# Performance work log

Hardware: AMD Instinct MI355X
Metric: run time of the kernel (lower is better)

Reference implementation:

```python
import jax, jax.numpy as jnp
import numpy as np

# Uniform ragged-segment sizes (ptr[i] = i * size)
B = 1024    # num graphs in batch
NT = 128    # tasks per graph
NV = 128    # vehicles per graph
NR = 16     # RSUs per graph
D = 64      # embed_dim
H = 32      # power-head hidden
NTGT = NR + NV
NEG = -1e9  # masked_fill value from the torch code


def setup_inputs() -> dict:
    key = jax.random.key(0)
    ks = jax.random.split(key, 10)
    return {
        "task_node_emb": jax.random.normal(ks[0], (B * NT, D), jnp.float32),
        "task_global_emb": jax.random.normal(ks[1], (B, D), jnp.float32),
        "veh_emb": jax.random.normal(ks[2], (B * NV, D), jnp.float32),
        "rsu_emb": jax.random.normal(ks[3], (B * NR, D), jnp.float32),
        "task_mask": jax.random.randint(ks[4], (B * NT,), 0, 2).astype(bool),
        "target_mask": jax.random.randint(ks[5], (B * NT, NTGT), 0, 2).astype(bool),
        "W1": jax.random.normal(ks[6], (2 * D, H), jnp.float32) * 0.1,
        "b1": jnp.zeros((H,), jnp.float32),
        "W2": jax.random.normal(ks[7], (H, 1), jnp.float32) * 0.1,
        "b2": jnp.zeros((1,), jnp.float32),
    }


def reference(task_node_emb, task_global_emb, veh_emb, rsu_emb,
              task_mask, target_mask, W1, b1, W2, b2):
    # Reshape flat ragged storage into uniform per-graph segments
    t = task_node_emb.reshape(B, NT, D)
    v = veh_emb.reshape(B, NV, D)
    r = rsu_emb.reshape(B, NR, D)

    # targets = cat([rsu, veh]) per graph; scores = task @ targets^T / sqrt(D)
    targets = jnp.concatenate([r, v], axis=1)              # [B, NTGT, D]
    scores = jnp.einsum('btd,bkd->btk', t, targets) / jnp.sqrt(jnp.float32(D))

    # masked_fill(~task_mask.unsqueeze(1), -1e9)
    tm = task_mask.reshape(B, NT, 1)
    scores = jnp.where(tm, scores, NEG)
    # masked_fill(~target_mask, -1e9) (same fill value, order irrelevant)
    tg = target_mask.reshape(B, NT, NTGT)
    scores = jnp.where(tg, scores, NEG)

    # flatten per graph; uniform lengths => pad_sequence is a no-op reshape
    padded_logits = scores.reshape(B, NT * NTGT)

    # power head on [task_global ; first vehicle emb of each graph]
    p_feat = jnp.concatenate([task_global_emb, v[:, 0, :]], axis=1)  # [B, 2D]
    h = jax.nn.relu(p_feat @ W1 + b1)
    power = jax.nn.sigmoid(h @ W2 + b2)                    # [B, 1]

    return padded_logits, power
```

## Files before the change

kernel.cpp:

```cpp
#include <hip/hip_runtime.h>

#define NB      1024
#define NT_     128
#define NV_     128
#define NR_     16
#define D_      64
#define H_      32
#define NTGT_   144
#define SCG     18432
#define PWR_OFF 18874368
#define NEGV    (-1e9f)
#define EPAD    148
#define EWAVE   (8 * EPAD)
#define NSB     2048

typedef __attribute__((ext_vector_type(8))) short  short8;
typedef __attribute__((ext_vector_type(4))) float  floatx4;

__device__ __forceinline__ unsigned int f2bf_pack(float lo, float hi) {
    unsigned int ul = __float_as_uint(lo);
    ul += 0x7FFFu + ((ul >> 16) & 1u);
    unsigned int uh = __float_as_uint(hi);
    uh += 0x7FFFu + ((uh >> 16) & 1u);
    return (ul >> 16) | (uh & 0xFFFF0000u);
}

extern "C" __global__ void __launch_bounds__(256, 8)
thy_fused(const float* __restrict__ tEmb,
          const float* __restrict__ gEmb,
          const float* __restrict__ vEmb,
          const float* __restrict__ rEmb,
          const int* __restrict__ tMask,
          const int* __restrict__ gMask,
          const float* __restrict__ W1,
          const float* __restrict__ b1,
          const float* __restrict__ W2,
          const float* __restrict__ b2,
          float* __restrict__ out)
{
    __shared__ __align__(16) unsigned char smem[18944];
    const int tid = threadIdx.x;
    const int blk = blockIdx.x;

    if (blk < NSB) {
        const int b    = blk >> 1;
        const int half = blk & 1;
        const int lane = tid & 63;
        const int w    = tid >> 6;
        const int ln   = lane & 15;
        const int kg   = lane >> 4;

        const float* arow_p = tEmb + ((size_t)b * NT_ + half * 64 + w * 16 + ln) * D_;
        float4 fa0 = *(const float4*)(arow_p + kg * 8);
        float4 fa1 = *(const float4*)(arow_p + kg * 8 + 4);
        float4 fb0 = *(const float4*)(arow_p + 32 + kg * 8);
        float4 fb1 = *(const float4*)(arow_p + 32 + kg * 8 + 4);

        {
            const float4* rs = (const float4*)(rEmb + (size_t)b * (NR_ * D_));
            const float4* vs = (const float4*)(vEmb + (size_t)b * (NV_ * D_));
            #pragma unroll
            for (int it = 0; it < 9; ++it) {
                int m = tid + it * 256;
                int row = m >> 4;
                float4 v = (row < 16) ? rs[m] : vs[m - 256];
                int cb  = (m & 15) << 3;
                int ad  = row * 128 + (cb ^ ((row & 7) << 4));
                uint2 p;
                p.x = f2bf_pack(v.x, v.y);
                p.y = f2bf_pack(v.z, v.w);
                *(uint2*)(smem + ad) = p;
            }
        }

        union { unsigned int u[4]; short8 s8; } A0, A1;
        A0.u[0] = f2bf_pack(fa0.x, fa0.y); A0.u[1] = f2bf_pack(fa0.z, fa0.w);
        A0.u[2] = f2bf_pack(fa1.x, fa1.y); A0.u[3] = f2bf_pack(fa1.z, fa1.w);
        A1.u[0] = f2bf_pack(fb0.x, fb0.y); A1.u[1] = f2bf_pack(fb0.z, fb0.w);
        A1.u[2] = f2bf_pack(fb1.x, fb1.y); A1.u[3] = f2bf_pack(fb1.z, fb1.w);

        __syncthreads();

        floatx4 acc[9] = {};
        #pragma unroll
        for (int s = 0; s < 2; ++s) {
            const int cb = s * 64 + kg * 16;
            const short8 av = (s == 0) ? A0.s8 : A1.s8;
            #pragma unroll
            for (int tn = 0; tn < 9; ++tn) {
                int row = tn * 16 + ln;
                short8 bb = *(const short8*)(smem + row * 128 + (cb ^ ((row & 7) << 4)));
                acc[tn] = __builtin_amdgcn_mfma_f32_16x16x32_bf16(av, bb, acc[tn], 0, 0, 0);
            }
        }

        __syncthreads();
        float* sc = (float*)smem;
        const int wbase = w * EWAVE;
        const size_t obase = (size_t)b * SCG;
        const int rbase = half * 64 + w * 16;

        #pragma unroll
        for (int p = 0; p < 2; ++p) {
            if ((kg >> 1) == p) {
                const int lr = (kg & 1) * 4;
                #pragma unroll
                for (int tn = 0; tn < 9; ++tn) {
                    #pragma unroll
                    for (int j = 0; j < 4; ++j) {
                        sc[wbase + (lr + j) * EPAD + tn * 16 + ln] = acc[tn][j] * 0.125f;
                    }
                }
            }
            #pragma unroll
            for (int u = 0; u < 5; ++u) {
                int chunk = lane + u * 64;
                if (chunk < 288) {
                    int row = chunk / 36;
                    int c4  = chunk - row * 36;
                    floatx4 sv = *(const floatx4*)(sc + wbase + row * EPAD + c4 * 4);
                    int r    = rbase + p * 8 + row;
                    int grow = b * NT_ + r;
                    floatx4 ov;
                    if (tMask[grow] != 0) {
                        int4 gm = *(const int4*)(gMask + (size_t)grow * NTGT_ + c4 * 4);
                        ov[0] = gm.x ? sv[0] : NEGV;
                        ov[1] = gm.y ? sv[1] : NEGV;
                        ov[2] = gm.z ? sv[2] : NEGV;
                        ov[3] = gm.w ? sv[3] : NEGV;
                    } else {
                        ov[0] = NEGV; ov[1] = NEGV; ov[2] = NEGV; ov[3] = NEGV;
                    }
                    __builtin_nontemporal_store(ov,
                        (floatx4*)(out + obase + (size_t)r * NTGT_ + c4 * 4));
                }
            }
        }
    } else {
        float* W1s = (float*)smem;
        #pragma unroll
        for (int it = 0; it < 4; ++it)
            ((float4*)W1s)[tid + it * 256] = ((const float4*)W1)[tid + it * 256];
        __syncthreads();

        const int gl = tid >> 3;
        const int jg = tid & 7;
        const int g  = (blk - NSB) * 32 + gl;
        const int j0 = jg * 4;

        floatx4 h;
        {
            float4 bb = *(const float4*)(b1 + j0);
            h[0] = bb.x; h[1] = bb.y; h[2] = bb.z; h[3] = bb.w;
        }
        const float4* fA = (const float4*)(gEmb + (size_t)g * D_);
        const float4* fB = (const float4*)(vEmb + (size_t)g * (NV_ * D_));
        #pragma unroll
        for (int i4 = 0; i4 < 16; ++i4) {
            float4 fv = fA[i4];
            float fr[4] = {fv.x, fv.y, fv.z, fv.w};
            #pragma unroll
            for (int rr = 0; rr < 4; ++rr) {
                float4 wv = *(const float4*)(W1s + ((i4 * 4 + rr) * H_) + j0);
                h[0] += fr[rr] * wv.x; h[1] += fr[rr] * wv.y;
                h[2] += fr[rr] * wv.z; h[3] += fr[rr] * wv.w;
            }
        }
        #pragma unroll
        for (int i4 = 0; i4 < 16; ++i4) {
            float4 fv = fB[i4];
            float fr[4] = {fv.x, fv.y, fv.z, fv.w};
            #pragma unroll
            for (int rr = 0; rr < 4; ++rr) {
                float4 wv = *(const float4*)(W1s + ((64 + i4 * 4 + rr) * H_) + j0);
                h[0] += fr[rr] * wv.x; h[1] += fr[rr] * wv.y;
                h[2] += fr[rr] * wv.z; h[3] += fr[rr] * wv.w;
            }
        }
        float4 w2v = *(const float4*)(W2 + j0);
        float p = fmaxf(h[0], 0.f) * w2v.x + fmaxf(h[1], 0.f) * w2v.y +
                  fmaxf(h[2], 0.f) * w2v.z + fmaxf(h[3], 0.f) * w2v.w;
        p += __shfl_xor(p, 1);
        p += __shfl_xor(p, 2);
        p += __shfl_xor(p, 4);
        if (jg == 0) {
            p += b2[0];
            out[PWR_OFF + g] = 1.0f / (1.0f + expf(-p));
        }
    }
}

extern "C" void kernel_launch(void* const* d_in, const int* in_sizes, int n_in,
                              void* d_out, int out_size, void* d_ws, size_t ws_size,
                              hipStream_t stream) {
    const float* tEmb = (const float*)d_in[0];
    const float* gEmb = (const float*)d_in[1];
    const float* vEmb = (const float*)d_in[2];
    const float* rEmb = (const float*)d_in[3];
    const int* tMask = (const int*)d_in[4];
    const int* gMask = (const int*)d_in[5];
    const float* W1 = (const float*)d_in[6];
    const float* b1 = (const float*)d_in[7];
    const float* W2 = (const float*)d_in[8];
    const float* b2 = (const float*)d_in[9];
    float* out = (float*)d_out;

    hipLaunchKernelGGL(thy_fused, dim3(NSB + 32), dim3(256), 0, stream,
                       tEmb, gEmb, vEmb, rEmb, tMask, gMask, W1, b1, W2, b2, out);
}
```

Baseline: 39.13 us.

## Swap MFMA operands to store accumulators directly and drop LDS epilogue staging

Swaps the A/B operands of the MFMA so each lane's accumulator holds four consecutive target columns of one task row. Results can then be masked and written straight from registers, with no LDS transpose, extra barrier or padded staging buffer. The block-to-graph mapping also changes so both halves of a graph land in different blocks far apart in launch order. The trade-off is that each lane now writes 16-byte pieces scattered across rows instead of wave-contiguous row segments, so store and mask-load coalescing gets worse.

```diff
diff --git a/kernel.cpp b/kernel.cpp
--- a/kernel.cpp
+++ b/kernel.cpp
@@ -10,8 +10,6 @@
 #define SCG     18432
 #define PWR_OFF 18874368
 #define NEGV    (-1e9f)
-#define EPAD    148
-#define EWAVE   (8 * EPAD)
 #define NSB     2048
 
 typedef __attribute__((ext_vector_type(8))) short  short8;
@@ -38,19 +36,23 @@
           const float* __restrict__ b2,
           float* __restrict__ out)
 {
-    __shared__ __align__(16) unsigned char smem[18944];
+    __shared__ __align__(16) unsigned char smem[18432];
     const int tid = threadIdx.x;
     const int blk = blockIdx.x;
 
     if (blk < NSB) {
-        const int b    = blk >> 1;
-        const int half = blk & 1;
+        const int b    = blk & 1023;
+        const int half = blk >> 10;
         const int lane = tid & 63;
         const int w    = tid >> 6;
         const int ln   = lane & 15;
         const int kg   = lane >> 4;
 
-        const float* arow_p = tEmb + ((size_t)b * NT_ + half * 64 + w * 16 + ln) * D_;
+        const int r    = half * 64 + w * 16 + ln;
+        const int grow = b * NT_ + r;
+        const int tm   = tMask[grow];
+
+        const float* arow_p = tEmb + ((size_t)b * NT_ + r) * D_;
         float4 fa0 = *(const float4*)(arow_p + kg * 8);
         float4 fa1 = *(const float4*)(arow_p + kg * 8 + 4);
         float4 fb0 = *(const float4*)(arow_p + 32 + kg * 8);
@@ -90,50 +92,29 @@
             for (int tn = 0; tn < 9; ++tn) {
                 int row = tn * 16 + ln;
                 short8 bb = *(const short8*)(smem + row * 128 + (cb ^ ((row & 7) << 4)));
-                acc[tn] = __builtin_amdgcn_mfma_f32_16x16x32_bf16(av, bb, acc[tn], 0, 0, 0);
+                acc[tn] = __builtin_amdgcn_mfma_f32_16x16x32_bf16(bb, av, acc[tn], 0, 0, 0);
             }
         }
 
-        __syncthreads();
-        float* sc = (float*)smem;
-        const int wbase = w * EWAVE;
-        const size_t obase = (size_t)b * SCG;
-        const int rbase = half * 64 + w * 16;
-
-        #pragma unroll
-        for (int p = 0; p < 2; ++p) {
-            if ((kg >> 1) == p) {
-                const int lr = (kg & 1) * 4;
-                #pragma unroll
-                for (int tn = 0; tn < 9; ++tn) {
-                    #pragma unroll
-                    for (int j = 0; j < 4; ++j) {
-                        sc[wbase + (lr + j) * EPAD + tn * 16 + ln] = acc[tn][j] * 0.125f;
-                    }
-                }
+        float* orow = out + (size_t)b * SCG + (size_t)r * NTGT_ + kg * 4;
+        if (tm != 0) {
+            const int* gmp = gMask + (size_t)grow * NTGT_ + kg * 4;
+            #pragma unroll
+            for (int tn = 0; tn < 9; ++tn) {
+                int4 gm = *(const int4*)(gmp + tn * 16);
+                floatx4 ov;
+                ov[0] = gm.x ? acc[tn][0] * 0.125f : NEGV;
+                ov[1] = gm.y ? acc[tn][1] * 0.125f : NEGV;
+                ov[2] = gm.z ? acc[tn][2] * 0.125f : NEGV;
+                ov[3] = gm.w ? acc[tn][3] * 0.125f : NEGV;
+                __builtin_nontemporal_store(ov, (floatx4*)(orow + tn * 16));
             }
+        } else {
+            floatx4 ov;
+            ov[0] = NEGV; ov[1] = NEGV; ov[2] = NEGV; ov[3] = NEGV;
             #pragma unroll
-            for (int u = 0; u < 5; ++u) {
-                int chunk = lane + u * 64;
-                if (chunk < 288) {
-                    int row = chunk / 36;
-                    int c4  = chunk - row * 36;
-                    floatx4 sv = *(const floatx4*)(sc + wbase + row * EPAD + c4 * 4);
-                    int r    = rbase + p * 8 + row;
-                    int grow = b * NT_ + r;
-                    floatx4 ov;
-                    if (tMask[grow] != 0) {
-                        int4 gm = *(const int4*)(gMask + (size_t)grow * NTGT_ + c4 * 4);
-                        ov[0] = gm.x ? sv[0] : NEGV;
-                        ov[1] = gm.y ? sv[1] : NEGV;
-                        ov[2] = gm.z ? sv[2] : NEGV;
-                        ov[3] = gm.w ? sv[3] : NEGV;
-                    } else {
-                        ov[0] = NEGV; ov[1] = NEGV; ov[2] = NEGV; ov[3] = NEGV;
-                    }
-                    __builtin_nontemporal_store(ov,
-                        (floatx4*)(out + obase + (size_t)r * NTGT_ + c4 * 4));
-                }
+            for (int tn = 0; tn < 9; ++tn) {
+                __builtin_nontemporal_store(ov, (floatx4*)(orow + tn * 16));
             }
         }
     } else {
```

After: 47.32 us. 20.9% more time.

## Process one graph per 512-thread block and fold power head into it

Applied to the files above, without the earlier changes.

Each block now handles a whole graph (all 128 tasks, 8 waves) instead of half a graph, so the 144 target rows are loaded and converted to bf16 once per graph rather than twice. The separate power-head blocks are removed, and wave 0 of each graph block computes that graph's power output with a per-lane dot product read directly from global W1. This halves target staging traffic and removes the tail blocks, at the cost of larger LDS use per block, fewer blocks, and some serial tail work on wave 0.

```diff
diff --git a/kernel.cpp b/kernel.cpp
--- a/kernel.cpp
+++ b/kernel.cpp
@@ -12,7 +12,6 @@
 #define NEGV    (-1e9f)
 #define EPAD    148
 #define EWAVE   (8 * EPAD)
-#define NSB     2048
 
 typedef __attribute__((ext_vector_type(8))) short  short8;
 typedef __attribute__((ext_vector_type(4))) float  floatx4;
@@ -25,7 +24,7 @@
     return (ul >> 16) | (uh & 0xFFFF0000u);
 }
 
-extern "C" __global__ void __launch_bounds__(256, 8)
+extern "C" __global__ void __launch_bounds__(512, 8)
 thy_fused(const float* __restrict__ tEmb,
           const float* __restrict__ gEmb,
           const float* __restrict__ vEmb,
@@ -38,30 +37,27 @@
           const float* __restrict__ b2,
           float* __restrict__ out)
 {
-    __shared__ __align__(16) unsigned char smem[18944];
-    const int tid = threadIdx.x;
-    const int blk = blockIdx.x;
+    __shared__ __align__(16) unsigned char smem[37888];
+    const int tid  = threadIdx.x;
+    const int b    = blockIdx.x;
+    const int lane = tid & 63;
+    const int w    = tid >> 6;
+    const int ln   = lane & 15;
+    const int kg   = lane >> 4;
 
-    if (blk < NSB) {
-        const int b    = blk >> 1;
-        const int half = blk & 1;
-        const int lane = tid & 63;
-        const int w    = tid >> 6;
-        const int ln   = lane & 15;
-        const int kg   = lane >> 4;
+    const float* arow_p = tEmb + ((size_t)b * NT_ + w * 16 + ln) * D_;
+    float4 fa0 = *(const float4*)(arow_p + kg * 8);
+    float4 fa1 = *(const float4*)(arow_p + kg * 8 + 4);
+    float4 fb0 = *(const float4*)(arow_p + 32 + kg * 8);
+    float4 fb1 = *(const float4*)(arow_p + 32 + kg * 8 + 4);
 
-        const float* arow_p = tEmb + ((size_t)b * NT_ + half * 64 + w * 16 + ln) * D_;
-        float4 fa0 = *(const float4*)(arow_p + kg * 8);
-        float4 fa1 = *(const float4*)(arow_p + kg * 8 + 4);
-        float4 fb0 = *(const float4*)(arow_p + 32 + kg * 8);
-        float4 fb1 = *(const float4*)(arow_p + 32 + kg * 8 + 4);
-
-        {
-            const float4* rs = (const float4*)(rEmb + (size_t)b * (NR_ * D_));
-            const float4* vs = (const float4*)(vEmb + (size_t)b * (NV_ * D_));
-            #pragma unroll
-            for (int it = 0; it < 9; ++it) {
-                int m = tid + it * 256;
+    {
+        const float4* rs = (const float4*)(rEmb + (size_t)b * (NR_ * D_));
+        const float4* vs = (const float4*)(vEmb + (size_t)b * (NV_ * D_));
+        #pragma unroll
+        for (int it = 0; it < 5; ++it) {
+            int m = tid + it * 512;
+            if (m < 2304) {
                 int row = m >> 4;
                 float4 v = (row < 16) ? rs[m] : vs[m - 256];
                 int cb  = (m & 15) << 3;
@@ -72,121 +68,91 @@
                 *(uint2*)(smem + ad) = p;
             }
         }
+    }
 
-        union { unsigned int u[4]; short8 s8; } A0, A1;
-        A0.u[0] = f2bf_pack(fa0.x, fa0.y); A0.u[1] = f2bf_pack(fa0.z, fa0.w);
-        A0.u[2] = f2bf_pack(fa1.x, fa1.y); A0.u[3] = f2bf_pack(fa1.z, fa1.w);
-        A1.u[0] = f2bf_pack(fb0.x, fb0.y); A1.u[1] = f2bf_pack(fb0.z, fb0.w);
-        A1.u[2] = f2bf_pack(fb1.x, fb1.y); A1.u[3] = f2bf_pack(fb1.z, fb1.w);
+    union { unsigned int u[4]; short8 s8; } A0, A1;
+    A0.u[0] = f2bf_pack(fa0.x, fa0.y); A0.u[1] = f2bf_pack(fa0.z, fa0.w);
+    A0.u[2] = f2bf_pack(fa1.x, fa1.y); A0.u[3] = f2bf_pack(fa1.z, fa1.w);
+    A1.u[0] = f2bf_pack(fb0.x, fb0.y); A1.u[1] = f2bf_pack(fb0.z, fb0.w);
+    A1.u[2] = f2bf_pack(fb1.x, fb1.y); A1.u[3] = f2bf_pack(fb1.z, fb1.w);
 
-        __syncthreads();
+    __syncthreads();
 
-        floatx4 acc[9] = {};
+    floatx4 acc[9] = {};
+    #pragma unroll
+    for (int s = 0; s < 2; ++s) {
+        const int cb = s * 64 + kg * 16;
+        const short8 av = (s == 0) ? A0.s8 : A1.s8;
         #pragma unroll
-        for (int s = 0; s < 2; ++s) {
-            const int cb = s * 64 + kg * 16;
-            const short8 av = (s == 0) ? A0.s8 : A1.s8;
+        for (int tn = 0; tn < 9; ++tn) {
+            int row = tn * 16 + ln;
+            short8 bb = *(const short8*)(smem + row * 128 + (cb ^ ((row & 7) << 4)));
+            acc[tn] = __builtin_amdgcn_mfma_f32_16x16x32_bf16(av, bb, acc[tn], 0, 0, 0);
+        }
+    }
+
+    __syncthreads();
+    float* sc = (float*)smem;
+    const int wbase = w * EWAVE;
+    const size_t obase = (size_t)b * SCG;
+    const int rbase = w * 16;
+
+    #pragma unroll
+    for (int p = 0; p < 2; ++p) {
+        if ((kg >> 1) == p) {
+            const int lr = (kg & 1) * 4;
             #pragma unroll
             for (int tn = 0; tn < 9; ++tn) {
-                int row = tn * 16 + ln;
-                short8 bb = *(const short8*)(smem + row * 128 + (cb ^ ((row & 7) << 4)));
-                acc[tn] = __builtin_amdgcn_mfma_f32_16x16x32_bf16(av, bb, acc[tn], 0, 0, 0);
-            }
-        }
-
-        __syncthreads();
-        float* sc = (float*)smem;
-        const int wbase = w * EWAVE;
-        const size_t obase = (size_t)b * SCG;
-        const int rbase = half * 64 + w * 16;
-
-        #pragma unroll
-        for (int p = 0; p < 2; ++p) {
-            if ((kg >> 1) == p) {
-                const int lr = (kg & 1) * 4;
                 #pragma unroll
-                for (int tn = 0; tn < 9; ++tn) {
-                    #pragma unroll
-                    for (int j = 0; j < 4; ++j) {
-                        sc[wbase + (lr + j) * EPAD + tn * 16 + ln] = acc[tn][j] * 0.125f;
-                    }
-                }
-            }
-            #pragma unroll
-            for (int u = 0; u < 5; ++u) {
-                int chunk = lane + u * 64;
-                if (chunk < 288) {
-                    int row = chunk / 36;
-                    int c4  = chunk - row * 36;
-                    floatx4 sv = *(const floatx4*)(sc + wbase + row * EPAD + c4 * 4);
-                    int r    = rbase + p * 8 + row;
-                    int grow = b * NT_ + r;
-                    floatx4 ov;
-                    if (tMask[grow] != 0) {
-                        int4 gm = *(const int4*)(gMask + (size_t)grow * NTGT_ + c4 * 4);
-                        ov[0] = gm.x ? sv[0] : NEGV;
-                        ov[1] = gm.y ? sv[1] : NEGV;
-                        ov[2] = gm.z ? sv[2] : NEGV;
-                        ov[3] = gm.w ? sv[3] : NEGV;
-                    } else {
-                        ov[0] = NEGV; ov[1] = NEGV; ov[2] = NEGV; ov[3] = NEGV;
-                    }
-                    __builtin_nontemporal_store(ov,
-                        (floatx4*)(out + obase + (size_t)r * NTGT_ + c4 * 4));
+                for (int j = 0; j < 4; ++j) {
+                    sc[wbase + (lr + j) * EPAD + tn * 16 + ln] = acc[tn][j] * 0.125f;
                 }
             }
         }
-    } else {
-        float* W1s = (float*)smem;
         #pragma unroll
-        for (int it = 0; it < 4; ++it)
-            ((float4*)W1s)[tid + it * 256] = ((const float4*)W1)[tid + it * 256];
-        __syncthreads();
-
-        const int gl = tid >> 3;
-        const int jg = tid & 7;
-        const int g  = (blk - NSB) * 32 + gl;
-        const int j0 = jg * 4;
-
-        floatx4 h;
-        {
-            float4 bb = *(const float4*)(b1 + j0);
-            h[0] = bb.x; h[1] = bb.y; h[2] = bb.z; h[3] = bb.w;
-        }
-        const float4* fA = (const float4*)(gEmb + (size_t)g * D_);
-        const float4* fB = (const float4*)(vEmb + (size_t)g * (NV_ * D_));
-        #pragma unroll
-        for (int i4 = 0; i4 < 16; ++i4) {
-            float4 fv = fA[i4];
-            float fr[4] = {fv.x, fv.y, fv.z, fv.w};
-            #pragma unroll
-            for (int rr = 0; rr < 4; ++rr) {
-                float4 wv = *(const float4*)(W1s + ((i4 * 4 + rr) * H_) + j0);
-                h[0] += fr[rr] * wv.x; h[1] += fr[rr] * wv.y;
-                h[2] += fr[rr] * wv.z; h[3] += fr[rr] * wv.w;
+        for (int u = 0; u < 5; ++u) {
+            int chunk = lane + u * 64;
+            if (chunk < 288) {
+                int row = chunk / 36;
+                int c4  = chunk - row * 36;
+                floatx4 sv = *(const floatx4*)(sc + wbase + row * EPAD + c4 * 4);
+                int r    = rbase + p * 8 + row;
+                int grow = b * NT_ + r;
+                floatx4 ov;
+                if (tMask[grow] != 0) {
+                    int4 gm = *(const int4*)(gMask + (size_t)grow * NTGT_ + c4 * 4);
+                    ov[0] = gm.x ? sv[0] : NEGV;
+                    ov[1] = gm.y ? sv[1] : NEGV;
+                    ov[2] = gm.z ? sv[2] : NEGV;
+                    ov[3] = gm.w ? sv[3] : NEGV;
+                } else {
+                    ov[0] = NEGV; ov[1] = NEGV; ov[2] = NEGV; ov[3] = NEGV;
+                }
+                __builtin_nontemporal_store(ov,
+                    (floatx4*)(out + obase + (size_t)r * NTGT_ + c4 * 4));
             }
         }
+    }
+
+    if (w == 0) {
+        const int j  = lane & 31;
+        const int hf = lane >> 5;
+        const float* fp = (hf == 0) ? (gEmb + (size_t)b * D_)
+                                    : (vEmb + (size_t)b * (NV_ * D_));
+        const float* wp = W1 + (size_t)hf * 64 * H_ + j;
+        float s = 0.f;
         #pragma unroll
-        for (int i4 = 0; i4 < 16; ++i4) {
-            float4 fv = fB[i4];
-            float fr[4] = {fv.x, fv.y, fv.z, fv.w};
-            #pragma unroll
-            for (int rr = 0; rr < 4; ++rr) {
-                float4 wv = *(const float4*)(W1s + ((64 + i4 * 4 + rr) * H_) + j0);
-                h[0] += fr[rr] * wv.x; h[1] += fr[rr] * wv.y;
-                h[2] += fr[rr] * wv.z; h[3] += fr[rr] * wv.w;
-            }
-        }
-        float4 w2v = *(const float4*)(W2 + j0);
-        float p = fmaxf(h[0], 0.f) * w2v.x + fmaxf(h[1], 0.f) * w2v.y +
-                  fmaxf(h[2], 0.f) * w2v.z + fmaxf(h[3], 0.f) * w2v.w;
-        p += __shfl_xor(p, 1);
-        p += __shfl_xor(p, 2);
-        p += __shfl_xor(p, 4);
-        if (jg == 0) {
-            p += b2[0];
-            out[PWR_OFF + g] = 1.0f / (1.0f + expf(-p));
-        }
+        for (int i = 0; i < 64; ++i)
+            s += fp[i] * wp[i * H_];
+        s += __shfl_xor(s, 32);
+        float t = fmaxf(s + b1[j], 0.f) * W2[j];
+        t += __shfl_xor(t, 1);
+        t += __shfl_xor(t, 2);
+        t += __shfl_xor(t, 4);
+        t += __shfl_xor(t, 8);
+        t += __shfl_xor(t, 16);
+        if (lane == 0)
+            out[PWR_OFF + b] = 1.0f / (1.0f + expf(-(t + b2[0])));
     }
 }
 
@@ -205,6 +171,6 @@
     const float* b2 = (const float*)d_in[9];
     float* out = (float*)d_out;
 
-    hipLaunchKernelGGL(thy_fused, dim3(NSB + 32), dim3(256), 0, stream,
+    hipLaunchKernelGGL(thy_fused, dim3(NB), dim3(512), 0, stream,
                        tEmb, gEmb, vEmb, rEmb, tMask, gMask, W1, b1, W2, b2, out);
 }
```

After: 36.59 us. 6.5% less time.
